# Performance work log

Hardware: AMD Instinct MI355X
Metric: run time of the kernel (lower is better)

The kernel has to match this reference:

```python
import jax, jax.numpy as jnp
import numpy as np
import math

D_MODEL = 1024
N_HEADS = 16
D_FF = 4096
D_K = D_MODEL // N_HEADS
B, S = 2, 2048
EPS = 1e-5


def _linear_params(key, fan_in, fan_out):
    kw, kb = jax.random.split(key)
    bound = 1.0 / math.sqrt(fan_in)
    W = jax.random.uniform(kw, (fan_out, fan_in), jnp.float32, -bound, bound)
    b = jax.random.uniform(kb, (fan_out,), jnp.float32, -bound, bound)
    return W, b


def setup_inputs() -> dict:
    key = jax.random.key(0)
    ks = jax.random.split(key, 8)
    x = jax.random.normal(ks[0], (B, S, D_MODEL), jnp.float32)
    # causal mask, broadcast over batch and heads; 0 -> masked
    mask = jnp.tril(jnp.ones((S, S), jnp.int32))[None, None, :, :]
    wq, bq = _linear_params(ks[1], D_MODEL, D_MODEL)
    wk, bk = _linear_params(ks[2], D_MODEL, D_MODEL)
    wv, bv = _linear_params(ks[3], D_MODEL, D_MODEL)
    wo, bo = _linear_params(ks[4], D_MODEL, D_MODEL)
    w1, b1 = _linear_params(ks[5], D_MODEL, D_FF)
    w2, b2 = _linear_params(ks[6], D_FF, D_MODEL)
    g1 = jnp.ones((D_MODEL,), jnp.float32)
    be1 = jnp.zeros((D_MODEL,), jnp.float32)
    g2 = jnp.ones((D_MODEL,), jnp.float32)
    be2 = jnp.zeros((D_MODEL,), jnp.float32)
    return dict(x=x, mask=mask, wq=wq, bq=bq, wk=wk, bk=bk, wv=wv, bv=bv,
                wo=wo, bo=bo, w1=w1, b1=b1, w2=w2, b2=b2,
                g1=g1, be1=be1, g2=g2, be2=be2)


def _layernorm(x, g, b):
    mu = jnp.mean(x, axis=-1, keepdims=True)
    var = jnp.mean(jnp.square(x - mu), axis=-1, keepdims=True)
    return (x - mu) * jax.lax.rsqrt(var + EPS) * g + b


def reference(x, mask, wq, bq, wk, bk, wv, bv, wo, bo, w1, b1, w2, b2, g1, be1, g2, be2):
    Bsz, Sl, _ = x.shape
    def heads(t):  # [B,S,D] -> [B,H,S,d_k]
        return t.reshape(Bsz, Sl, N_HEADS, D_K).transpose(0, 2, 1, 3)
    Q = heads(x @ wq.T + bq)
    K = heads(x @ wk.T + bk)
    V = heads(x @ wv.T + bv)
    scores = jnp.einsum('bhqd,bhkd->bhqk', Q, K) / math.sqrt(D_K)
    scores = jnp.where(mask == 0, jnp.float32(-1e9), scores)
    attn = jax.nn.softmax(scores, axis=-1)
    out = jnp.einsum('bhqk,bhkd->bhqd', attn, V)
    out = out.transpose(0, 2, 1, 3).reshape(Bsz, Sl, D_MODEL)
    attn_out = out @ wo.T + bo
    h = _layernorm(x + attn_out, g1, be1)  # dropout is identity in eval
    ff = jax.nn.relu(h @ w1.T + b1) @ w2.T + b2
    return _layernorm(h + ff, g2, be2)
```

## Files before the change

kernel.cpp:

```cpp
#include <hip/hip_runtime.h>
#include <hip/hip_bf16.h>


using f32x4 = __attribute__((ext_vector_type(4))) float;
using s16x8 = __attribute__((ext_vector_type(8))) short;

constexpr int D_MODEL = 1024;
constexpr int D_FF    = 4096;
constexpr int DK      = 64;
constexpr int BB      = 2;
constexpr int SS      = 2048;
constexpr int NTOK    = BB * SS;

#define QSCALE 0.18033688011112042f

__device__ __forceinline__ ushort f2bf(float f) {
    unsigned u = __float_as_uint(f);
    u += 0x7fffu + ((u >> 16) & 1u);
    return (ushort)(u >> 16);
}

__device__ __forceinline__ float bflo(uint v) { return __uint_as_float(v << 16); }
__device__ __forceinline__ float bfhi(uint v) { return __uint_as_float(v & 0xffff0000u); }

__device__ __forceinline__ float ex2(float x) {
    float r;
    asm("v_exp_f32 %0, %1" : "=v"(r) : "v"(x));
    return r;
}

__device__ __forceinline__ void gload_lds16(const void* g, void* l) {
    __builtin_amdgcn_global_load_lds(
        (const __attribute__((address_space(1))) void*)g,
        (__attribute__((address_space(3))) void*)l, 16, 0, 0);
}

__device__ __forceinline__ void wait_vm4() {
    asm volatile("s_waitcnt vmcnt(4)" ::: "memory");
    __builtin_amdgcn_sched_barrier(0);
}
__device__ __forceinline__ void wait_vm0() {
    asm volatile("s_waitcnt vmcnt(0)" ::: "memory");
    __builtin_amdgcn_sched_barrier(0);
}
__device__ __forceinline__ void wait_lgkm0() {
    asm volatile("s_waitcnt lgkmcnt(0)" ::: "memory");
    __builtin_amdgcn_sched_barrier(0);
}

struct CvtArgs { const float* src[7]; ushort* dst[7]; };

__global__ __launch_bounds__(256) void cvt_all(CvtArgs a) {
    constexpr long S[8] = {0L<<20, 1L<<20, 2L<<20, 3L<<20,
                           4L<<20, 8L<<20, 12L<<20, 16L<<20};
    long i = ((long)blockIdx.x * 256 + threadIdx.x) * 4;
    int s = 0;
#pragma unroll
    for (int j = 1; j < 7; ++j) if (i >= S[j]) s = j;
    long off = i - S[s];
    float4 v = *(const float4*)(a.src[s] + off);
    ushort4 o;
    o.x = f2bf(v.x); o.y = f2bf(v.y); o.z = f2bf(v.z); o.w = f2bf(v.w);
    *(ushort4*)(a.dst[s] + off) = o;
}

__global__ __launch_bounds__(512, 2) void gemm256_relu(
        const ushort* __restrict__ A, const ushort* __restrict__ Wt,
        const float* __restrict__ bias, ushort* __restrict__ C,
        int M, int N, int K) {
    __shared__ __align__(16) char Als[2][2][128 * 128];
    __shared__ __align__(16) char Bls[2][2][128 * 128];

    const int nwg = (int)gridDim.x;
    const int id  = (int)blockIdx.x;
    const int sw  = (id & 7) * (nwg >> 3) + (id >> 3);
    const int gx  = N >> 8;
    const int bx  = sw % gx, by = sw / gx;
    const int bm0 = by << 8, bn0 = bx << 8;

    const int t  = threadIdx.x;
    const int l  = t & 63;
    const int w  = t >> 6;
    const int li = l & 15, g = l >> 4;
    const int wm = w >> 2, wn = w & 3;

    const int srow  = w * 8 + (l >> 3);
    const int scolb = (l & 7) * 16;
    const int svz   = (scolb ^ ((srow & 4) << 3)) >> 1;
    const int nk    = K >> 6;

    auto stA = [&](int buf, int half, int kt) {
        if (kt >= nk) return;
        const ushort* src = A + (size_t)(bm0 + half * 128 + srow) * K + kt * 64 + svz;
        char* dst = Als[buf][half] + w * 1024;
        gload_lds16(src, dst);
        gload_lds16(src + (size_t)64 * K, dst + 8192);
    };
    auto stB = [&](int buf, int half, int kt) {
        if (kt >= nk) return;
        const ushort* src = Wt + (size_t)(bn0 + half * 128 + srow) * K + kt * 64 + svz;
        char* dst = Bls[buf][half] + w * 1024;
        gload_lds16(src, dst);
        gload_lds16(src + (size_t)64 * K, dst + 8192);
    };

    const int rdsw = (li & 4) << 3;

    f32x4 acc[8][4];
#pragma unroll
    for (int m = 0; m < 8; ++m)
#pragma unroll
        for (int n = 0; n < 4; ++n)
            acc[m][n] = (f32x4){0.f, 0.f, 0.f, 0.f};

    auto ldA2 = [&](int buf, int q, s16x8 af[2][2]) {
#pragma unroll
        for (int m2 = 0; m2 < 2; ++m2)
#pragma unroll
            for (int kk = 0; kk < 2; ++kk)
                af[m2][kk] = *(const s16x8*)(Als[buf][wm] +
                    ((q * 2 + m2) * 16 + li) * 128 + ((kk * 64 + g * 16) ^ rdsw));
    };
    auto ldB8 = [&](int buf, s16x8 bfr[4][2]) {
#pragma unroll
        for (int nf = 0; nf < 4; ++nf)
#pragma unroll
            for (int kk = 0; kk < 2; ++kk)
                bfr[nf][kk] = *(const s16x8*)(Bls[buf][wn >> 1] +
                    ((wn & 1) * 64 + nf * 16 + li) * 128 + ((kk * 64 + g * 16) ^ rdsw));
    };
    auto mfmaq = [&](int q, s16x8 af[2][2], s16x8 bfr[4][2], int wm_mode) {
        __builtin_amdgcn_s_barrier();
        wait_lgkm0();
        __builtin_amdgcn_s_setprio(1);
#pragma unroll
        for (int m2 = 0; m2 < 2; ++m2)
#pragma unroll
            for (int nf = 0; nf < 4; ++nf)
#pragma unroll
            for (int kk = 0; kk < 2; ++kk)
                acc[q * 2 + m2][nf] = __builtin_amdgcn_mfma_f32_16x16x32_bf16(
                    af[m2][kk], bfr[nf][kk], acc[q * 2 + m2][nf], 0, 0, 0);
        __builtin_amdgcn_s_setprio(0);
        if (wm_mode == 4) wait_vm4();
        else if (wm_mode == 0) wait_vm0();
        __builtin_amdgcn_s_barrier();
    };

    stB(0, 0, 0); stB(0, 1, 0);
    stA(0, 0, 0); stA(0, 1, 0);
    stB(1, 0, 1); stB(1, 1, 1);
    wait_vm4();
    __builtin_amdgcn_s_barrier();

    const int ni = nk >> 1;
    for (int i = 0; i < ni; ++i) {
        const int t0 = 2 * i;
        const bool last = (i == ni - 1);
        {
            s16x8 bfr[4][2];
            { ldB8(0, bfr); s16x8 af[2][2]; ldA2(0, 0, af);
              stA(1, 0, t0 + 1);                      mfmaq(0, af, bfr, -1); }
            { s16x8 af[2][2]; ldA2(0, 1, af);
              stA(1, 1, t0 + 1); stB(0, 0, t0 + 2);   mfmaq(1, af, bfr, -1); }
            { s16x8 af[2][2]; ldA2(0, 2, af);
              stB(0, 1, t0 + 2);                      mfmaq(2, af, bfr, -1); }
            { s16x8 af[2][2]; ldA2(0, 3, af);
                                                      mfmaq(3, af, bfr, last ? 0 : 4); }
        }
        {
            s16x8 bfr[4][2];
            { ldB8(1, bfr); s16x8 af[2][2]; ldA2(1, 0, af);
              stA(0, 0, t0 + 2);                      mfmaq(0, af, bfr, -1); }
            { s16x8 af[2][2]; ldA2(1, 1, af);
              stA(0, 1, t0 + 2);                      mfmaq(1, af, bfr, -1); }
            { s16x8 af[2][2]; ldA2(1, 2, af);
              stB(1, 0, t0 + 3);                      mfmaq(2, af, bfr, -1); }
            { s16x8 af[2][2]; ldA2(1, 3, af);
              stB(1, 1, t0 + 3);
                                                      mfmaq(3, af, bfr, last ? -1 : 4); }
        }
    }

#pragma unroll
    for (int mf = 0; mf < 8; ++mf) {
        int row0 = bm0 + wm * 128 + mf * 16 + g * 4;
#pragma unroll
        for (int nf = 0; nf < 4; ++nf) {
            int col = bn0 + wn * 64 + nf * 16 + li;
            float bsv = bias[col];
#pragma unroll
            for (int r = 0; r < 4; ++r) {
                float v = fmaxf(acc[mf][nf][r] + bsv, 0.f);
                C[(size_t)(row0 + r) * N + col] = f2bf(v);
            }
        }
    }
}

template <bool RELU, bool OUTBF16>
__global__ __launch_bounds__(256, 2) void gemm_bt(
        const ushort* __restrict__ A, const ushort* __restrict__ W,
        const float* __restrict__ bias,
        void* __restrict__ Cout, int M, int N, int Klen, int ldk, int gx, int splitk) {
    __shared__ __align__(16) char Asb[2][128 * 128];
    __shared__ __align__(16) char Bsb[2][128 * 128];

    const int nwg = (int)gridDim.x;
    const int id  = (int)blockIdx.x;
    const int sw  = (id & 7) * (nwg >> 3) + (id >> 3);
    const int tps = nwg / splitk;
    const int s   = sw / tps;
    const int rem = sw - s * tps;
    const int bx  = rem % gx, by = rem / gx;

    const int t  = threadIdx.x;
    const int l  = t & 63;
    const int w  = t >> 6;
    const int wr = w >> 1, wc = w & 1;
    const int li = l & 15, g = l >> 4;
    const int bm0 = by << 7;
    const int bn0 = bx << 7;
    const int kbase = s * Klen;

    f32x4 acc[4][4];
#pragma unroll
    for (int m = 0; m < 4; ++m)
#pragma unroll
        for (int n = 0; n < 4; ++n)
            acc[m][n] = (f32x4){0.f, 0.f, 0.f, 0.f};

    const int rsub = l >> 3, slot = l & 7;
    const int swzel = (((slot * 16) ^ (rsub << 4)) >> 1);

    auto stage = [&](int buf, int k0) {
#pragma unroll
        for (int i = 0; i < 4; ++i) {
            const int rbase = i * 32 + w * 8;
            gload_lds16(A + (size_t)(bm0 + rbase + rsub) * ldk + kbase + k0 + swzel,
                        Asb[buf] + rbase * 128);
            gload_lds16(W + (size_t)(bn0 + rbase + rsub) * ldk + kbase + k0 + swzel,
                        Bsb[buf] + rbase * 128);
        }
    };

    const int nk = Klen >> 6;
    stage(0, 0);
    __syncthreads();

    for (int tt = 0; tt < nk; ++tt) {
        const int cur = tt & 1;
        if (tt + 1 < nk) stage(cur ^ 1, (tt + 1) << 6);
#pragma unroll
        for (int ks = 0; ks < 2; ++ks) {
            s16x8 af[4], bfr[4];
#pragma unroll
            for (int m = 0; m < 4; ++m) {
                int row = wr * 64 + m * 16 + li;
                af[m] = *(const s16x8*)(Asb[cur] + row * 128 + (((ks * 4 + g) * 16) ^ ((row & 7) << 4)));
            }
#pragma unroll
            for (int n = 0; n < 4; ++n) {
                int row = wc * 64 + n * 16 + li;
                bfr[n] = *(const s16x8*)(Bsb[cur] + row * 128 + (((ks * 4 + g) * 16) ^ ((row & 7) << 4)));
            }
            __builtin_amdgcn_s_setprio(1);
#pragma unroll
            for (int m = 0; m < 4; ++m)
#pragma unroll
                for (int n = 0; n < 4; ++n)
                    acc[m][n] = __builtin_amdgcn_mfma_f32_16x16x32_bf16(af[m], bfr[n], acc[m][n], 0, 0, 0);
            __builtin_amdgcn_s_setprio(0);
        }
        __syncthreads();
    }

    const bool dobias = (s == 0);
    float* Cf = (float*)Cout + (size_t)s * M * N;
#pragma unroll
    for (int m = 0; m < 4; ++m) {
        int row0 = bm0 + wr * 64 + m * 16 + g * 4;
#pragma unroll
        for (int n = 0; n < 4; ++n) {
            int col = bn0 + wc * 64 + n * 16 + li;
            float bsv = dobias ? bias[col] : 0.f;
#pragma unroll
            for (int r = 0; r < 4; ++r) {
                float v = acc[m][n][r] + bsv;
                if (RELU) v = fmaxf(v, 0.f);
                size_t idx = (size_t)(row0 + r) * N + col;
                if (OUTBF16) ((ushort*)Cout)[idx] = f2bf(v);
                else         Cf[idx] = v;
            }
        }
    }
}

__global__ __launch_bounds__(256, 2) void gemm_qkvt(
        const ushort* __restrict__ xb, const ushort* __restrict__ wqkb,
        const ushort* __restrict__ wvb,
        const float* __restrict__ bq, const float* __restrict__ bk,
        const float* __restrict__ bv,
        ushort* __restrict__ QKb, ushort* __restrict__ VtG) {
    __shared__ __align__(16) char Asb[2][128 * 128];
    __shared__ __align__(16) char Bsb[2][128 * 128];

    const int id = (int)blockIdx.x;
    const int sw = (id & 7) * 96 + (id >> 3);
    const bool vt = (sw >= 512);
    int bx, by, N;
    const ushort *A, *W;
    if (!vt) { bx = sw % 16;          by = sw / 16;          A = xb;  W = wqkb; N = 2048; }
    else     { int s2 = sw - 512; bx = s2 % 32; by = s2 / 32; A = wvb; W = xb;  N = 4096; }

    const int t  = threadIdx.x;
    const int l  = t & 63;
    const int w  = t >> 6;
    const int wr = w >> 1, wc = w & 1;
    const int li = l & 15, g = l >> 4;
    const int bm0 = by << 7;
    const int bn0 = bx << 7;

    f32x4 acc[4][4];
#pragma unroll
    for (int m = 0; m < 4; ++m)
#pragma unroll
        for (int n = 0; n < 4; ++n)
            acc[m][n] = (f32x4){0.f, 0.f, 0.f, 0.f};

    const int rsub = l >> 3, slot = l & 7;
    const int swzel = (((slot * 16) ^ (rsub << 4)) >> 1);

    auto stage = [&](int buf, int k0) {
#pragma unroll
        for (int i = 0; i < 4; ++i) {
            const int rbase = i * 32 + w * 8;
            gload_lds16(A + (size_t)(bm0 + rbase + rsub) * 1024 + k0 + swzel,
                        Asb[buf] + rbase * 128);
            gload_lds16(W + (size_t)(bn0 + rbase + rsub) * 1024 + k0 + swzel,
                        Bsb[buf] + rbase * 128);
        }
    };

    stage(0, 0);
    __syncthreads();

    for (int tt = 0; tt < 16; ++tt) {
        const int cur = tt & 1;
        if (tt + 1 < 16) stage(cur ^ 1, (tt + 1) << 6);
#pragma unroll
        for (int ks = 0; ks < 2; ++ks) {
            s16x8 af[4], bfr[4];
#pragma unroll
            for (int m = 0; m < 4; ++m) {
                int row = wr * 64 + m * 16 + li;
                af[m] = *(const s16x8*)(Asb[cur] + row * 128 + (((ks * 4 + g) * 16) ^ ((row & 7) << 4)));
            }
#pragma unroll
            for (int n = 0; n < 4; ++n) {
                int row = wc * 64 + n * 16 + li;
                bfr[n] = *(const s16x8*)(Bsb[cur] + row * 128 + (((ks * 4 + g) * 16) ^ ((row & 7) << 4)));
            }
            __builtin_amdgcn_s_setprio(1);
#pragma unroll
            for (int m = 0; m < 4; ++m)
#pragma unroll
                for (int n = 0; n < 4; ++n)
                    acc[m][n] = __builtin_amdgcn_mfma_f32_16x16x32_bf16(af[m], bfr[n], acc[m][n], 0, 0, 0);
            __builtin_amdgcn_s_setprio(0);
        }
        __syncthreads();
    }

#pragma unroll
    for (int m = 0; m < 4; ++m) {
        int row0 = bm0 + wr * 64 + m * 16 + g * 4;
#pragma unroll
        for (int n = 0; n < 4; ++n) {
            int col = bn0 + wc * 64 + n * 16 + li;
            if (!vt) {
                float bsv = (col < 1024) ? bq[col] : bk[col - 1024];
                float sc  = (col < 1024) ? QSCALE : 1.f;
#pragma unroll
                for (int r = 0; r < 4; ++r) {
                    float v = (acc[m][n][r] + bsv) * sc;
                    QKb[(size_t)(row0 + r) * 2048 + col] = f2bf(v);
                }
            } else {
#pragma unroll
                for (int r = 0; r < 4; ++r) {
                    float v = acc[m][n][r] + bv[row0 + r];
                    VtG[(size_t)(row0 + r) * 4096 + col] = f2bf(v);
                }
            }
        }
    }
}

__global__ __launch_bounds__(256, 4) void attn_kernel(
        const ushort* __restrict__ QKb, const ushort* __restrict__ VtG,
        ushort* __restrict__ po, float* __restrict__ ml) {
    __shared__ __align__(16) char Ks[2][64 * 128];
    __shared__ __align__(16) char Vs[2][64 * 128];
    __shared__ __align__(16) char Ps[4][16 * 128];

    const int t  = threadIdx.x;
    const int l  = t & 63;
    const int w  = t >> 6;
    const int li = l & 15, g = l >> 4;
    const int bx = (int)blockIdx.x;
    const int h  = blockIdx.y;
    const int z  = (int)blockIdx.z;
    const int b    = z & 1;
    const int half = z >> 1;

    const ushort* Kp = QKb + (size_t)(b * SS) * 2048 + 1024 + h * DK;
    const ushort* Vp = VtG + (size_t)(h * DK) * NTOK + b * SS;

    const int rsub = l >> 3, slot = l & 7;
    const int swzsrc = (slot * 16) ^ (rsub << 4);

    auto stage = [&](int buf, int kt) {
#pragma unroll
        for (int c = 0; c < 2; ++c) {
            int row0 = (w + c * 4) * 8;
            gload_lds16((const char*)(Kp + (size_t)(kt + row0 + rsub) * 2048) + swzsrc,
                        Ks[buf] + row0 * 128);
            gload_lds16((const char*)(Vp + (size_t)(row0 + rsub) * NTOK + kt) + swzsrc,
                        Vs[buf] + row0 * 128);
        }
    };

    char* Pw = Ps[w];
    const int rswz = (li & 7) << 4;

    for (int ss = 0; ss < 2; ++ss) {
        const int stripe = ss ? bx : (SS / 64 - 1 - bx);
        const int qb = stripe * 64;
        const int qw = qb + w * 16;

        const ushort* Qp = QKb + (size_t)(b * SS + qw) * 2048 + h * DK;
        s16x8 qf[2];
#pragma unroll
        for (int ds = 0; ds < 2; ++ds)
            qf[ds] = *(const s16x8*)(Qp + li * 2048 + ds * 32 + g * 8);

        f32x4 o[4];
#pragma unroll
        for (int d = 0; d < 4; ++d) o[d] = (f32x4){0.f, 0.f, 0.f, 0.f};
        float m_ = -1e30f, ls = 0.f;

        const int ntt  = stripe + 1;
        const int tbeg = half ? (ntt >> 1) : 0;
        const int tend = half ? ntt : (ntt >> 1);
        const int ntH  = tend - tbeg;

        if (ntH > 0) {
            stage(0, tbeg * 64);
            __syncthreads();

            for (int tt = 0; tt < ntH; ++tt) {
                const int kt = (tbeg + tt) * 64;
                const int cur = tt & 1;
                if (tt + 1 < ntH) stage(cur ^ 1, kt + 64);

                f32x4 sa[4];
#pragma unroll
                for (int ks = 0; ks < 4; ++ks) sa[ks] = (f32x4){0.f, 0.f, 0.f, 0.f};
#pragma unroll
                for (int ks = 0; ks < 4; ++ks) {
                    int row = ks * 16 + li;
#pragma unroll
                    for (int ds = 0; ds < 2; ++ds) {
                        s16x8 kf = *(const s16x8*)(Ks[cur] + row * 128 + ((ds * 64 + g * 16) ^ rswz));
                        __builtin_amdgcn_s_setprio(1);
                        sa[ks] = __builtin_amdgcn_mfma_f32_16x16x32_bf16(kf, qf[ds], sa[ks], 0, 0, 0);
                        __builtin_amdgcn_s_setprio(0);
                    }
                }

                const bool maskt = (tbeg + tt == ntt - 1);
                float p[4][4];
                float pmax = -1e30f;
#pragma unroll
                for (int ks = 0; ks < 4; ++ks)
#pragma unroll
                    for (int r = 0; r < 4; ++r) {
                        float sv = sa[ks][r];
                        if (maskt && (kt + ks * 16 + g * 4 + r > qw + li)) sv = -1e30f;
                        p[ks][r] = sv;
                        pmax = fmaxf(pmax, sv);
                    }

                if (!__all(pmax <= m_ + 11.5f)) {
                    float mx = fmaxf(pmax, __shfl_xor(pmax, 16));
                    mx = fmaxf(mx, __shfl_xor(mx, 32));
                    float nm = fmaxf(m_, mx);
                    float fs = ex2(m_ - nm);
                    m_ = nm;
                    ls *= fs;
                    float fsr[4];
#pragma unroll
                    for (int r = 0; r < 4; ++r) fsr[r] = __shfl(fs, g * 4 + r);
#pragma unroll
                    for (int d = 0; d < 4; ++d)
#pragma unroll
                        for (int r = 0; r < 4; ++r) o[d][r] *= fsr[r];
                }
                float rs = 0.f;
#pragma unroll
                for (int ks = 0; ks < 4; ++ks)
#pragma unroll
                    for (int r = 0; r < 4; ++r) {
                        p[ks][r] = ex2(p[ks][r] - m_);
                        rs += p[ks][r];
                    }
                rs += __shfl_xor(rs, 16);
                rs += __shfl_xor(rs, 32);
                ls += rs;

#pragma unroll
                for (int ks = 0; ks < 4; ++ks) {
                    uint u0, u1;
                    asm("v_cvt_pk_bf16_f32 %0, %1, %2" : "=v"(u0) : "v"(p[ks][0]), "v"(p[ks][1]));
                    asm("v_cvt_pk_bf16_f32 %0, %1, %2" : "=v"(u1) : "v"(p[ks][2]), "v"(p[ks][3]));
                    uint2 uv; uv.x = u0; uv.y = u1;
                    *(uint2*)(Pw + li * 128 + ((ks * 32 + g * 8) ^ rswz)) = uv;
                }

                s16x8 pf[2];
#pragma unroll
                for (int ks2 = 0; ks2 < 2; ++ks2)
                    pf[ks2] = *(const s16x8*)(Pw + li * 128 + ((ks2 * 64 + g * 16) ^ rswz));
#pragma unroll
                for (int dblk = 0; dblk < 4; ++dblk) {
                    int vrow = dblk * 16 + li;
#pragma unroll
                    for (int ks2 = 0; ks2 < 2; ++ks2) {
                        s16x8 vf = *(const s16x8*)(Vs[cur] + vrow * 128 + ((ks2 * 64 + g * 16) ^ rswz));
                        __builtin_amdgcn_s_setprio(1);
                        o[dblk] = __builtin_amdgcn_mfma_f32_16x16x32_bf16(pf[ks2], vf, o[dblk], 0, 0, 0);
                        __builtin_amdgcn_s_setprio(0);
                    }
                }
                __syncthreads();
            }
        }

#pragma unroll
        for (int r = 0; r < 4; ++r) {
            ushort* pp = po + ((((size_t)(half * 2 + b)) * SS + qw + g * 4 + r) * 16 + h) * 64;
#pragma unroll
            for (int dblk = 0; dblk < 4; ++dblk)
                pp[dblk * 16 + li] = f2bf(o[dblk][r]);
        }
        if (l < 16) {
            size_t mrow = (((size_t)(half * 2 + b)) * SS + qw + l) * 16 + h;
            ml[mrow * 2]     = m_;
            ml[mrow * 2 + 1] = ls;
        }
    }
}

__global__ __launch_bounds__(256) void attn_combine(
        const ushort* __restrict__ po, const float* __restrict__ ml,
        ushort* __restrict__ ctx) {
    const int idx = blockIdx.x * 256 + threadIdx.x;
    const int row = idx >> 4;
    const int d4  = (idx & 15) * 4;
    const int HR  = 2 * SS * 16;

    float m0 = ml[(size_t)row * 2],        l0 = ml[(size_t)row * 2 + 1];
    float m1 = ml[(size_t)(HR + row) * 2], l1 = ml[(size_t)(HR + row) * 2 + 1];
    float mx = fmaxf(m0, m1);
    float w0 = ex2(m0 - mx), w1 = ex2(m1 - mx);
    float inv = 1.0f / (l0 * w0 + l1 * w1);

    uint2 a = *(const uint2*)(po + (size_t)row * 64 + d4);
    uint2 c = *(const uint2*)(po + (size_t)(HR + row) * 64 + d4);
    float v0 = (bflo(a.x) * w0 + bflo(c.x) * w1) * inv;
    float v1 = (bfhi(a.x) * w0 + bfhi(c.x) * w1) * inv;
    float v2 = (bflo(a.y) * w0 + bflo(c.y) * w1) * inv;
    float v3 = (bfhi(a.y) * w0 + bfhi(c.y) * w1) * inv;
    ushort4 o;
    o.x = f2bf(v0); o.y = f2bf(v1); o.z = f2bf(v2); o.w = f2bf(v3);
    *(ushort4*)(ctx + (size_t)(row >> 4) * 1024 + (row & 15) * 64 + d4) = o;
}

template <bool WBF, bool X3>
__global__ __launch_bounds__(256) void ln_fused(
        const float* __restrict__ xa, const float* __restrict__ xb,
        const float* __restrict__ xc,
        const float* __restrict__ gamma, const float* __restrict__ beta,
        float* __restrict__ outf, ushort* __restrict__ outb) {
    const int row = blockIdx.x;
    const int t   = threadIdx.x;
    const size_t off = (size_t)row * D_MODEL + t * 4;
    float4 a = *(const float4*)(xa + off);
    float4 c = *(const float4*)(xb + off);
    float z0 = a.x + c.x, z1 = a.y + c.y, z2 = a.z + c.z, z3 = a.w + c.w;
    if constexpr (X3) {
        float4 d = *(const float4*)(xc + off);
        z0 += d.x; z1 += d.y; z2 += d.z; z3 += d.w;
    }
    float sum = z0 + z1 + z2 + z3;
    float sq  = z0 * z0 + z1 * z1 + z2 * z2 + z3 * z3;
#pragma unroll
    for (int o = 1; o < 64; o <<= 1) {
        sum += __shfl_xor(sum, o);
        sq  += __shfl_xor(sq, o);
    }
    __shared__ float s1[4], s2[4];
    if ((t & 63) == 0) { s1[t >> 6] = sum; s2[t >> 6] = sq; }
    __syncthreads();
    float tot = s1[0] + s1[1] + s1[2] + s1[3];
    float tsq = s2[0] + s2[1] + s2[2] + s2[3];
    const float invn = 1.0f / (float)D_MODEL;
    float mu  = tot * invn;
    float var = tsq * invn - mu * mu;
    float rstd = rsqrtf(var + 1e-5f);
    float4 gv = *(const float4*)(gamma + t * 4);
    float4 bv = *(const float4*)(beta + t * 4);
    float y0 = (z0 - mu) * rstd * gv.x + bv.x;
    float y1 = (z1 - mu) * rstd * gv.y + bv.y;
    float y2 = (z2 - mu) * rstd * gv.z + bv.z;
    float y3 = (z3 - mu) * rstd * gv.w + bv.w;
    float4 y = {y0, y1, y2, y3};
    *(float4*)(outf + off) = y;
    if constexpr (WBF) {
        ushort4 u;
        u.x = f2bf(y0); u.y = f2bf(y1); u.z = f2bf(y2); u.w = f2bf(y3);
        *(ushort4*)(outb + off) = u;
    }
}

extern "C" void kernel_launch(void* const* d_in, const int* in_sizes, int n_in,
                              void* d_out, int out_size, void* d_ws, size_t ws_size,
                              hipStream_t stream) {
    const float* x   = (const float*)d_in[0];
    const float* wq  = (const float*)d_in[2];  const float* bq  = (const float*)d_in[3];
    const float* wk  = (const float*)d_in[4];  const float* bk  = (const float*)d_in[5];
    const float* wv  = (const float*)d_in[6];  const float* bv  = (const float*)d_in[7];
    const float* wo  = (const float*)d_in[8];  const float* bo  = (const float*)d_in[9];
    const float* w1  = (const float*)d_in[10]; const float* b1  = (const float*)d_in[11];
    const float* w2  = (const float*)d_in[12]; const float* b2  = (const float*)d_in[13];
    const float* g1  = (const float*)d_in[14]; const float* be1 = (const float*)d_in[15];
    const float* g2  = (const float*)d_in[16]; const float* be2 = (const float*)d_in[17];
    float* out = (float*)d_out;

    char* ws = (char*)d_ws;
    const size_t MB = 1u << 20;
    ushort* wqkb = (ushort*)(ws + 0 * MB);
    ushort* wvb  = (ushort*)(ws + 4 * MB);
    ushort* wob  = (ushort*)(ws + 6 * MB);
    ushort* w1b  = (ushort*)(ws + 8 * MB);
    ushort* w2b  = (ushort*)(ws + 16 * MB);
    ushort* xb   = (ushort*)(ws + 24 * MB);
    ushort* QKb  = (ushort*)(ws + 32 * MB);
    ushort* VtG  = (ushort*)(ws + 48 * MB);
    ushort* ctx  = (ushort*)(ws + 56 * MB);
    ushort* po   = (ushort*)(ws + 64 * MB);
    float*  ml   = (float*)(ws + 81 * MB);
    float*  p0   = (float*)(ws + 64 * MB);
    float*  p1   = (float*)(ws + 80 * MB);
    float*  h    = (float*)(ws + 96 * MB);
    ushort* hb   = (ushort*)(ws + 112 * MB);
    ushort* ffib = (ushort*)(ws + 24 * MB);

    CvtArgs ca;
    ca.src[0] = wq; ca.dst[0] = wqkb;
    ca.src[1] = wk; ca.dst[1] = wqkb + D_MODEL * D_MODEL;
    ca.src[2] = wv; ca.dst[2] = wvb;
    ca.src[3] = wo; ca.dst[3] = wob;
    ca.src[4] = w1; ca.dst[4] = w1b;
    ca.src[5] = w2; ca.dst[5] = w2b;
    ca.src[6] = x;  ca.dst[6] = xb;
    cvt_all<<<dim3(16384), dim3(256), 0, stream>>>(ca);

    dim3 blk(256);
    gemm_qkvt<<<dim3(768), blk, 0, stream>>>(xb, wqkb, wvb, bq, bk, bv, QKb, VtG);

    attn_kernel<<<dim3(SS / 128, 16, 2 * BB), blk, 0, stream>>>(QKb, VtG, po, ml);
    attn_combine<<<dim3(4096), blk, 0, stream>>>(po, ml, ctx);

    gemm_bt<false, false><<<dim3(512), blk, 0, stream>>>(
        ctx, wob, bo, p0, NTOK, D_MODEL, 512, D_MODEL, 8, 2);
    ln_fused<true, true><<<dim3(NTOK), blk, 0, stream>>>(x, p0, p1, g1, be1, h, hb);

    gemm256_relu<<<dim3(256), dim3(512), 0, stream>>>(hb, w1b, b1, ffib, NTOK, D_FF, D_MODEL);

    gemm_bt<false, false><<<dim3(512), blk, 0, stream>>>(
        ffib, w2b, b2, p0, NTOK, D_MODEL, 2048, D_FF, 8, 2);
    ln_fused<false, true><<<dim3(NTOK), blk, 0, stream>>>(h, p0, p1, g2, be2, out, nullptr);
}
```

Baseline: 236.1 us.

## Share K/V tiles between paired query stripes and remap blocks to XCDs

The attention kernel now processes its high and low query stripes together: each staged K/V tile is reused by both stripes when causally valid, instead of looping over the two stripes separately and reloading K/V for each. The key range is split between the two halves by interleaving even and odd tiles rather than contiguous halves. A 1D grid with an explicit XCD-aware mapping groups blocks that share the same head and batch onto the same XCD for L2 locality. This cuts K/V global and LDS loads, but doubles the register state for accumulators and Q fragments, which may pressure occupancy under the 4-block launch bound.

```diff
diff --git a/kernel.cpp b/kernel.cpp
--- a/kernel.cpp
+++ b/kernel.cpp
@@ -408,11 +408,16 @@
     const int l  = t & 63;
     const int w  = t >> 6;
     const int li = l & 15, g = l >> 4;
-    const int bx = (int)blockIdx.x;
-    const int h  = blockIdx.y;
-    const int z  = (int)blockIdx.z;
-    const int b    = z & 1;
-    const int half = z >> 1;
+
+    const int id   = (int)blockIdx.x;
+    const int xcd  = id & 7;
+    const int rest = id >> 3;
+    const int grp  = xcd + 8 * (rest >> 5);
+    const int k32  = rest & 31;
+    const int h    = grp >> 1;
+    const int b    = grp & 1;
+    const int bx   = k32 & 15;
+    const int half = k32 >> 4;
 
     const ushort* Kp = QKb + (size_t)(b * SS) * 2048 + 1024 + h * DK;
     const ushort* Vp = VtG + (size_t)(h * DK) * NTOK + b * SS;
@@ -434,131 +439,147 @@
     char* Pw = Ps[w];
     const int rswz = (li & 7) << 4;
 
-    for (int ss = 0; ss < 2; ++ss) {
-        const int stripe = ss ? bx : (SS / 64 - 1 - bx);
-        const int qb = stripe * 64;
-        const int qw = qb + w * 16;
-
-        const ushort* Qp = QKb + (size_t)(b * SS + qw) * 2048 + h * DK;
-        s16x8 qf[2];
-#pragma unroll
-        for (int ds = 0; ds < 2; ++ds)
-            qf[ds] = *(const s16x8*)(Qp + li * 2048 + ds * 32 + g * 8);
-
-        f32x4 o[4];
-#pragma unroll
-        for (int d = 0; d < 4; ++d) o[d] = (f32x4){0.f, 0.f, 0.f, 0.f};
-        float m_ = -1e30f, ls = 0.f;
-
-        const int ntt  = stripe + 1;
-        const int tbeg = half ? (ntt >> 1) : 0;
-        const int tend = half ? ntt : (ntt >> 1);
-        const int ntH  = tend - tbeg;
-
-        if (ntH > 0) {
-            stage(0, tbeg * 64);
-            __syncthreads();
-
-            for (int tt = 0; tt < ntH; ++tt) {
-                const int kt = (tbeg + tt) * 64;
-                const int cur = tt & 1;
-                if (tt + 1 < ntH) stage(cur ^ 1, kt + 64);
-
-                f32x4 sa[4];
-#pragma unroll
-                for (int ks = 0; ks < 4; ++ks) sa[ks] = (f32x4){0.f, 0.f, 0.f, 0.f};
-#pragma unroll
-                for (int ks = 0; ks < 4; ++ks) {
-                    int row = ks * 16 + li;
-#pragma unroll
-                    for (int ds = 0; ds < 2; ++ds) {
-                        s16x8 kf = *(const s16x8*)(Ks[cur] + row * 128 + ((ds * 64 + g * 16) ^ rswz));
-                        __builtin_amdgcn_s_setprio(1);
-                        sa[ks] = __builtin_amdgcn_mfma_f32_16x16x32_bf16(kf, qf[ds], sa[ks], 0, 0, 0);
-                        __builtin_amdgcn_s_setprio(0);
-                    }
-                }
-
-                const bool maskt = (tbeg + tt == ntt - 1);
-                float p[4][4];
-                float pmax = -1e30f;
-#pragma unroll
-                for (int ks = 0; ks < 4; ++ks)
-#pragma unroll
-                    for (int r = 0; r < 4; ++r) {
-                        float sv = sa[ks][r];
-                        if (maskt && (kt + ks * 16 + g * 4 + r > qw + li)) sv = -1e30f;
-                        p[ks][r] = sv;
-                        pmax = fmaxf(pmax, sv);
-                    }
-
-                if (!__all(pmax <= m_ + 11.5f)) {
-                    float mx = fmaxf(pmax, __shfl_xor(pmax, 16));
-                    mx = fmaxf(mx, __shfl_xor(mx, 32));
-                    float nm = fmaxf(m_, mx);
-                    float fs = ex2(m_ - nm);
-                    m_ = nm;
-                    ls *= fs;
-                    float fsr[4];
-#pragma unroll
-                    for (int r = 0; r < 4; ++r) fsr[r] = __shfl(fs, g * 4 + r);
-#pragma unroll
-                    for (int d = 0; d < 4; ++d)
-#pragma unroll
-                        for (int r = 0; r < 4; ++r) o[d][r] *= fsr[r];
-                }
-                float rs = 0.f;
-#pragma unroll
-                for (int ks = 0; ks < 4; ++ks)
-#pragma unroll
-                    for (int r = 0; r < 4; ++r) {
-                        p[ks][r] = ex2(p[ks][r] - m_);
-                        rs += p[ks][r];
-                    }
-                rs += __shfl_xor(rs, 16);
-                rs += __shfl_xor(rs, 32);
-                ls += rs;
-
-#pragma unroll
-                for (int ks = 0; ks < 4; ++ks) {
-                    uint u0, u1;
-                    asm("v_cvt_pk_bf16_f32 %0, %1, %2" : "=v"(u0) : "v"(p[ks][0]), "v"(p[ks][1]));
-                    asm("v_cvt_pk_bf16_f32 %0, %1, %2" : "=v"(u1) : "v"(p[ks][2]), "v"(p[ks][3]));
-                    uint2 uv; uv.x = u0; uv.y = u1;
-                    *(uint2*)(Pw + li * 128 + ((ks * 32 + g * 8) ^ rswz)) = uv;
-                }
-
-                s16x8 pf[2];
-#pragma unroll
-                for (int ks2 = 0; ks2 < 2; ++ks2)
-                    pf[ks2] = *(const s16x8*)(Pw + li * 128 + ((ks2 * 64 + g * 16) ^ rswz));
-#pragma unroll
-                for (int dblk = 0; dblk < 4; ++dblk) {
-                    int vrow = dblk * 16 + li;
-#pragma unroll
-                    for (int ks2 = 0; ks2 < 2; ++ks2) {
-                        s16x8 vf = *(const s16x8*)(Vs[cur] + vrow * 128 + ((ks2 * 64 + g * 16) ^ rswz));
-                        __builtin_amdgcn_s_setprio(1);
-                        o[dblk] = __builtin_amdgcn_mfma_f32_16x16x32_bf16(pf[ks2], vf, o[dblk], 0, 0, 0);
-                        __builtin_amdgcn_s_setprio(0);
-                    }
-                }
-                __syncthreads();
-            }
-        }
-
-#pragma unroll
-        for (int r = 0; r < 4; ++r) {
-            ushort* pp = po + ((((size_t)(half * 2 + b)) * SS + qw + g * 4 + r) * 16 + h) * 64;
-#pragma unroll
-            for (int dblk = 0; dblk < 4; ++dblk)
-                pp[dblk * 16 + li] = f2bf(o[dblk][r]);
-        }
-        if (l < 16) {
-            size_t mrow = (((size_t)(half * 2 + b)) * SS + qw + l) * 16 + h;
-            ml[mrow * 2]     = m_;
-            ml[mrow * 2 + 1] = ls;
-        }
+    const int hi  = SS / 64 - 1 - bx;
+    const int lo  = bx;
+    const int qwH = hi * 64 + w * 16;
+    const int qwL = lo * 64 + w * 16;
+
+    s16x8 qfH[2], qfL[2];
+    {
+        const ushort* QpH = QKb + (size_t)(b * SS + qwH) * 2048 + h * DK;
+        const ushort* QpL = QKb + (size_t)(b * SS + qwL) * 2048 + h * DK;
+#pragma unroll
+        for (int ds = 0; ds < 2; ++ds) {
+            qfH[ds] = *(const s16x8*)(QpH + li * 2048 + ds * 32 + g * 8);
+            qfL[ds] = *(const s16x8*)(QpL + li * 2048 + ds * 32 + g * 8);
+        }
+    }
+
+    f32x4 oH[4], oL[4];
+#pragma unroll
+    for (int d = 0; d < 4; ++d) {
+        oH[d] = (f32x4){0.f, 0.f, 0.f, 0.f};
+        oL[d] = (f32x4){0.f, 0.f, 0.f, 0.f};
+    }
+    float mH = -1e30f, lsH = 0.f, mL = -1e30f, lsL = 0.f;
+
+    auto process = [&](const s16x8 (&qf)[2], f32x4 (&o)[4], float& m_, float& ls,
+                       int j, int stripe, int qw, int cur) {
+        const int kt = j * 64;
+        f32x4 sa[4];
+#pragma unroll
+        for (int ks = 0; ks < 4; ++ks) sa[ks] = (f32x4){0.f, 0.f, 0.f, 0.f};
+#pragma unroll
+        for (int ks = 0; ks < 4; ++ks) {
+            int row = ks * 16 + li;
+#pragma unroll
+            for (int ds = 0; ds < 2; ++ds) {
+                s16x8 kf = *(const s16x8*)(Ks[cur] + row * 128 + ((ds * 64 + g * 16) ^ rswz));
+                __builtin_amdgcn_s_setprio(1);
+                sa[ks] = __builtin_amdgcn_mfma_f32_16x16x32_bf16(kf, qf[ds], sa[ks], 0, 0, 0);
+                __builtin_amdgcn_s_setprio(0);
+            }
+        }
+
+        const bool maskt = (j == stripe);
+        float p[4][4];
+        float pmax = -1e30f;
+#pragma unroll
+        for (int ks = 0; ks < 4; ++ks)
+#pragma unroll
+            for (int r = 0; r < 4; ++r) {
+                float sv = sa[ks][r];
+                if (maskt && (kt + ks * 16 + g * 4 + r > qw + li)) sv = -1e30f;
+                p[ks][r] = sv;
+                pmax = fmaxf(pmax, sv);
+            }
+
+        if (!__all(pmax <= m_ + 11.5f)) {
+            float mx = fmaxf(pmax, __shfl_xor(pmax, 16));
+            mx = fmaxf(mx, __shfl_xor(mx, 32));
+            float nm = fmaxf(m_, mx);
+            float fs = ex2(m_ - nm);
+            m_ = nm;
+            ls *= fs;
+            float fsr[4];
+#pragma unroll
+            for (int r = 0; r < 4; ++r) fsr[r] = __shfl(fs, g * 4 + r);
+#pragma unroll
+            for (int d = 0; d < 4; ++d)
+#pragma unroll
+                for (int r = 0; r < 4; ++r) o[d][r] *= fsr[r];
+        }
+        float rs = 0.f;
+#pragma unroll
+        for (int ks = 0; ks < 4; ++ks)
+#pragma unroll
+            for (int r = 0; r < 4; ++r) {
+                p[ks][r] = ex2(p[ks][r] - m_);
+                rs += p[ks][r];
+            }
+        rs += __shfl_xor(rs, 16);
+        rs += __shfl_xor(rs, 32);
+        ls += rs;
+
+#pragma unroll
+        for (int ks = 0; ks < 4; ++ks) {
+            uint u0, u1;
+            asm("v_cvt_pk_bf16_f32 %0, %1, %2" : "=v"(u0) : "v"(p[ks][0]), "v"(p[ks][1]));
+            asm("v_cvt_pk_bf16_f32 %0, %1, %2" : "=v"(u1) : "v"(p[ks][2]), "v"(p[ks][3]));
+            uint2 uv; uv.x = u0; uv.y = u1;
+            *(uint2*)(Pw + li * 128 + ((ks * 32 + g * 8) ^ rswz)) = uv;
+        }
+
+        s16x8 pf[2];
+#pragma unroll
+        for (int ks2 = 0; ks2 < 2; ++ks2)
+            pf[ks2] = *(const s16x8*)(Pw + li * 128 + ((ks2 * 64 + g * 16) ^ rswz));
+#pragma unroll
+        for (int dblk = 0; dblk < 4; ++dblk) {
+            int vrow = dblk * 16 + li;
+#pragma unroll
+            for (int ks2 = 0; ks2 < 2; ++ks2) {
+                s16x8 vf = *(const s16x8*)(Vs[cur] + vrow * 128 + ((ks2 * 64 + g * 16) ^ rswz));
+                __builtin_amdgcn_s_setprio(1);
+                o[dblk] = __builtin_amdgcn_mfma_f32_16x16x32_bf16(pf[ks2], vf, o[dblk], 0, 0, 0);
+                __builtin_amdgcn_s_setprio(0);
+            }
+        }
+    };
+
+    const int nt = ((hi - half) >> 1) + 1;
+    stage(0, half * 64);
+    __syncthreads();
+
+    for (int it = 0; it < nt; ++it) {
+        const int j   = half + 2 * it;
+        const int cur = it & 1;
+        if (it + 1 < nt) stage(cur ^ 1, j * 64 + 128);
+
+        process(qfH, oH, mH, lsH, j, hi, qwH, cur);
+        if (j <= lo)
+            process(qfL, oL, mL, lsL, j, lo, qwL, cur);
+
+        __syncthreads();
+    }
+
+#pragma unroll
+    for (int r = 0; r < 4; ++r) {
+        ushort* ppH = po + ((((size_t)(half * 2 + b)) * SS + qwH + g * 4 + r) * 16 + h) * 64;
+        ushort* ppL = po + ((((size_t)(half * 2 + b)) * SS + qwL + g * 4 + r) * 16 + h) * 64;
+#pragma unroll
+        for (int dblk = 0; dblk < 4; ++dblk) {
+            ppH[dblk * 16 + li] = f2bf(oH[dblk][r]);
+            ppL[dblk * 16 + li] = f2bf(oL[dblk][r]);
+        }
+    }
+    if (l < 16) {
+        size_t mrowH = (((size_t)(half * 2 + b)) * SS + qwH + l) * 16 + h;
+        ml[mrowH * 2]     = mH;
+        ml[mrowH * 2 + 1] = lsH;
+        size_t mrowL = (((size_t)(half * 2 + b)) * SS + qwL + l) * 16 + h;
+        ml[mrowL * 2]     = mL;
+        ml[mrowL * 2 + 1] = lsL;
     }
 }
 
@@ -680,7 +701,7 @@
     dim3 blk(256);
     gemm_qkvt<<<dim3(768), blk, 0, stream>>>(xb, wqkb, wvb, bq, bk, bv, QKb, VtG);
 
-    attn_kernel<<<dim3(SS / 128, 16, 2 * BB), blk, 0, stream>>>(QKb, VtG, po, ml);
+    attn_kernel<<<dim3(1024), blk, 0, stream>>>(QKb, VtG, po, ml);
     attn_combine<<<dim3(4096), blk, 0, stream>>>(po, ml, ctx);
 
     gemm_bt<false, false><<<dim3(512), blk, 0, stream>>>(
```

Measured after the change: 229.8 us. 2.7% less time.
